# Optimization experiments

Hardware: AMD Instinct MI355X
Metric: run time of the kernel (lower is better)

The kernel has to match this reference:

```python
import jax, jax.numpy as jnp
import numpy as np

E = 4_194_304
N_COMPANY = 100_000
N_CAUSE, N_COURT, N_RES = 200, 50, 10
D_CA, D_COURT, D_CATE = 12, 4, 4
D = D_CA + D_COURT + D_CATE  # 20


def setup_inputs() -> dict:
    key = jax.random.key(0)
    ks = jax.random.split(key, 10)
    cause_idx = jax.random.randint(ks[0], (E,), 0, N_CAUSE, dtype=jnp.int32)
    court_idx = jax.random.randint(ks[1], (E,), 0, N_COURT, dtype=jnp.int32)
    cate_idx = jax.random.randint(ks[2], (E,), 0, N_RES, dtype=jnp.int32)
    seg_ids = jnp.sort(jax.random.randint(ks[3], (E,), 0, N_COMPANY, dtype=jnp.int32))
    time_interval = jax.random.uniform(ks[4], (E,), dtype=jnp.float32) * 365.0
    # learned parameters (nn.Embedding default init ~ N(0,1); Linear ~ U)
    ca_table = jax.random.normal(ks[5], (N_CAUSE, D_CA), dtype=jnp.float32)
    court_table = jax.random.normal(ks[6], (N_COURT, D_COURT), dtype=jnp.float32)
    cate_table = jax.random.normal(ks[7], (N_RES, D_CATE), dtype=jnp.float32)
    lim = 1.0 / np.sqrt(D)
    proj_w = jax.random.uniform(ks[8], (D, D), dtype=jnp.float32, minval=-lim, maxval=lim)
    decay_w = jax.random.uniform(ks[9], (), dtype=jnp.float32, minval=0.5, maxval=1.5)
    return {
        "cause_idx": cause_idx, "court_idx": court_idx, "cate_idx": cate_idx,
        "seg_ids": seg_ids, "time_interval": time_interval,
        "ca_table": ca_table, "court_table": court_table, "cate_table": cate_table,
        "proj_w": proj_w, "decay_w": decay_w,
    }


def reference(cause_idx, court_idx, cate_idx, seg_ids, time_interval,
              ca_table, court_table, cate_table, proj_w, decay_w):
    # per-event categorical embedding gather -> [E, 20]
    risk = jnp.concatenate(
        [ca_table[cause_idx], court_table[court_idx], cate_table[cate_idx]], axis=1)
    # Decayer: learnable scale times inverse-log time decay
    decay = decay_w / jnp.log(jnp.e + time_interval)  # [E]
    # proj(decay * risk): Linear(20, 20, bias=False) -> x @ W^T
    y = jnp.einsum('ed,od->eo', decay[:, None] * risk, proj_w)
    # per-company sum reduction (the original Python loop over companies)
    com_emb = jax.ops.segment_sum(y, seg_ids, num_segments=N_COMPANY,
                                  indices_are_sorted=True)
    return com_emb
```

## Files before the change

kernel.cpp:

```cpp
#include <hip/hip_runtime.h>

#define NCOMP   100000
#define D_CA    12
#define D_COURT 4
#define D_CATE  4
#define D_TOT   20
#define NCAUSE  200
#define NCOURT  50
#define NRES    10
#define LPC     4

__global__ void seg_starts_kernel(const int* __restrict__ seg, int n_events,
                                  int* __restrict__ start) {
    int i = blockIdx.x * blockDim.x + threadIdx.x;
    if (i >= n_events) return;
    const int cur = seg[i];
    const int prev = (i == 0) ? -1 : seg[i - 1];
    for (int c = prev + 1; c <= cur; ++c) start[c] = i;
    if (i == n_events - 1) {
        for (int c = cur + 1; c <= NCOMP; ++c) start[c] = n_events;
    }
}

__global__ __launch_bounds__(256)
void company_emb_kernel(const int* __restrict__ cause_idx,
                        const int* __restrict__ court_idx,
                        const int* __restrict__ cate_idx,
                        const float* __restrict__ time_interval,
                        const float* __restrict__ ca_table,
                        const float* __restrict__ court_table,
                        const float* __restrict__ cate_table,
                        const float* __restrict__ proj_w,
                        const float* __restrict__ decay_w,
                        const int* __restrict__ start,
                        float* __restrict__ out) {
    __shared__ __align__(16) float lds_ca[NCAUSE * D_CA];
    __shared__ __align__(16) float lds_court[NCOURT * D_COURT];
    __shared__ __align__(16) float lds_cate[NRES * D_CATE];
    __shared__ __align__(16) float lds_w[D_TOT * D_TOT];

    for (int i = threadIdx.x; i < NCAUSE * D_CA; i += 256) lds_ca[i] = ca_table[i];
    for (int i = threadIdx.x; i < NCOURT * D_COURT; i += 256) lds_court[i] = court_table[i];
    for (int i = threadIdx.x; i < NRES * D_CATE; i += 256) lds_cate[i] = cate_table[i];
    for (int i = threadIdx.x; i < D_TOT * D_TOT; i += 256) lds_w[i] = proj_w[i];
    __syncthreads();

    const float dw = decay_w[0];
    const int tid = blockIdx.x * 256 + threadIdx.x;
    const int c = tid >> 2;
    const int sub = threadIdx.x & (LPC - 1);
    if (c >= NCOMP) return;

    const int s0 = start[c];
    const int s1 = start[c + 1];

    float acc[D_TOT];
#pragma unroll
    for (int d = 0; d < D_TOT; ++d) acc[d] = 0.0f;

    for (int i = s0 + sub; i < s1; i += LPC) {
        const int ca = cause_idx[i];
        const int co = court_idx[i];
        const int ct = cate_idx[i];
        const float t = time_interval[i];
        const float decay = __fdividef(dw, __logf(2.718281828459045f + t));

        const float4* car = (const float4*)(lds_ca + ca * D_CA);
        const float4 a0 = car[0];
        const float4 a1 = car[1];
        const float4 a2 = car[2];
        const float4 b0 = *(const float4*)(lds_court + co * D_COURT);
        const float4 c0 = *(const float4*)(lds_cate + ct * D_CATE);

        acc[0]  += decay * a0.x;  acc[1]  += decay * a0.y;
        acc[2]  += decay * a0.z;  acc[3]  += decay * a0.w;
        acc[4]  += decay * a1.x;  acc[5]  += decay * a1.y;
        acc[6]  += decay * a1.z;  acc[7]  += decay * a1.w;
        acc[8]  += decay * a2.x;  acc[9]  += decay * a2.y;
        acc[10] += decay * a2.z;  acc[11] += decay * a2.w;
        acc[12] += decay * b0.x;  acc[13] += decay * b0.y;
        acc[14] += decay * b0.z;  acc[15] += decay * b0.w;
        acc[16] += decay * c0.x;  acc[17] += decay * c0.y;
        acc[18] += decay * c0.z;  acc[19] += decay * c0.w;
    }

#pragma unroll
    for (int d = 0; d < D_TOT; ++d) {
        float v = acc[d];
        v += __shfl_xor(v, 1);
        v += __shfl_xor(v, 2);
        acc[d] = v;
    }

#pragma unroll
    for (int k = 0; k < 5; ++k) {
        const int o = sub * 5 + k;
        float s = 0.0f;
#pragma unroll
        for (int d = 0; d < D_TOT; ++d) s += acc[d] * lds_w[o * D_TOT + d];
        out[c * D_TOT + o] = s;
    }
}

extern "C" void kernel_launch(void* const* d_in, const int* in_sizes, int n_in,
                              void* d_out, int out_size, void* d_ws, size_t ws_size,
                              hipStream_t stream) {
    const int* cause_idx = (const int*)d_in[0];
    const int* court_idx = (const int*)d_in[1];
    const int* cate_idx  = (const int*)d_in[2];
    const int* seg_ids   = (const int*)d_in[3];
    const float* time_interval = (const float*)d_in[4];
    const float* ca_table      = (const float*)d_in[5];
    const float* court_table   = (const float*)d_in[6];
    const float* cate_table    = (const float*)d_in[7];
    const float* proj_w        = (const float*)d_in[8];
    const float* decay_w       = (const float*)d_in[9];
    float* out = (float*)d_out;
    const int n_events = in_sizes[0];

    int* start = (int*)d_ws;

    {
        const int blocks = (n_events + 255) / 256;
        seg_starts_kernel<<<blocks, 256, 0, stream>>>(seg_ids, n_events, start);
    }
    {
        const int groups = NCOMP;
        const int blocks = (groups * LPC + 255) / 256;
        company_emb_kernel<<<blocks, 256, 0, stream>>>(
            cause_idx, court_idx, cate_idx, time_interval,
            ca_table, court_table, cate_table, proj_w, decay_w,
            start, out);
    }
}
```

Measured before the change: 156.3 us.

## Fuse segment-start search into main kernel via per-block binary search

Removes the separate segment-start kernel, which read all of seg_ids and wrote a start array. Each block now binary-searches seg_ids for the boundaries of its 32 companies and keeps them in shared memory. Lanes per company go from 4 to 8, and the event loop is unrolled by two to keep more loads in flight. The cost is a serial chain of about 22 dependent global loads per block before any event work begins, plus a shuffle reduction stage widened to eight lanes.

```diff
diff --git a/kernel.cpp b/kernel.cpp
--- a/kernel.cpp
+++ b/kernel.cpp
@@ -8,93 +8,98 @@
 #define NCAUSE  200
 #define NCOURT  50
 #define NRES    10
-#define LPC     4
-
-__global__ void seg_starts_kernel(const int* __restrict__ seg, int n_events,
-                                  int* __restrict__ start) {
-    int i = blockIdx.x * blockDim.x + threadIdx.x;
-    if (i >= n_events) return;
-    const int cur = seg[i];
-    const int prev = (i == 0) ? -1 : seg[i - 1];
-    for (int c = prev + 1; c <= cur; ++c) start[c] = i;
-    if (i == n_events - 1) {
-        for (int c = cur + 1; c <= NCOMP; ++c) start[c] = n_events;
-    }
-}
+#define LPC     8
+#define CPB     32
 
 __global__ __launch_bounds__(256)
-void company_emb_kernel(const int* __restrict__ cause_idx,
-                        const int* __restrict__ court_idx,
-                        const int* __restrict__ cate_idx,
-                        const float* __restrict__ time_interval,
-                        const float* __restrict__ ca_table,
-                        const float* __restrict__ court_table,
-                        const float* __restrict__ cate_table,
-                        const float* __restrict__ proj_w,
-                        const float* __restrict__ decay_w,
-                        const int* __restrict__ start,
-                        float* __restrict__ out) {
+void fused_company_kernel(const int* __restrict__ cause_idx,
+                          const int* __restrict__ court_idx,
+                          const int* __restrict__ cate_idx,
+                          const int* __restrict__ seg_ids,
+                          const float* __restrict__ time_interval,
+                          const float* __restrict__ ca_table,
+                          const float* __restrict__ court_table,
+                          const float* __restrict__ cate_table,
+                          const float* __restrict__ proj_w,
+                          const float* __restrict__ decay_w,
+                          int n_events,
+                          float* __restrict__ out) {
     __shared__ __align__(16) float lds_ca[NCAUSE * D_CA];
     __shared__ __align__(16) float lds_court[NCOURT * D_COURT];
     __shared__ __align__(16) float lds_cate[NRES * D_CATE];
     __shared__ __align__(16) float lds_w[D_TOT * D_TOT];
+    __shared__ int lds_start[CPB + 1];
 
     for (int i = threadIdx.x; i < NCAUSE * D_CA; i += 256) lds_ca[i] = ca_table[i];
     for (int i = threadIdx.x; i < NCOURT * D_COURT; i += 256) lds_court[i] = court_table[i];
     for (int i = threadIdx.x; i < NRES * D_CATE; i += 256) lds_cate[i] = cate_table[i];
     for (int i = threadIdx.x; i < D_TOT * D_TOT; i += 256) lds_w[i] = proj_w[i];
+
+    if (threadIdx.x <= CPB) {
+        const int c = blockIdx.x * CPB + threadIdx.x;
+        int lo = 0, hi = n_events;
+        while (lo < hi) {
+            const int mid = (lo + hi) >> 1;
+            if (seg_ids[mid] < c) lo = mid + 1; else hi = mid;
+        }
+        lds_start[threadIdx.x] = lo;
+    }
     __syncthreads();
 
     const float dw = decay_w[0];
-    const int tid = blockIdx.x * 256 + threadIdx.x;
-    const int c = tid >> 2;
+    const int g   = threadIdx.x >> 3;
     const int sub = threadIdx.x & (LPC - 1);
-    if (c >= NCOMP) return;
-
-    const int s0 = start[c];
-    const int s1 = start[c + 1];
+    const int c   = blockIdx.x * CPB + g;
+    const int s0  = lds_start[g];
+    const int s1  = lds_start[g + 1];
 
     float acc[D_TOT];
 #pragma unroll
     for (int d = 0; d < D_TOT; ++d) acc[d] = 0.0f;
 
-    for (int i = s0 + sub; i < s1; i += LPC) {
-        const int ca = cause_idx[i];
-        const int co = court_idx[i];
-        const int ct = cate_idx[i];
-        const float t = time_interval[i];
-        const float decay = __fdividef(dw, __logf(2.718281828459045f + t));
+#define EV_BODY(I)                                                           \
+    {                                                                        \
+        const int   ca = cause_idx[I];                                       \
+        const int   co = court_idx[I];                                       \
+        const int   ct = cate_idx[I];                                        \
+        const float t  = time_interval[I];                                   \
+        const float dec = __fdividef(dw, __logf(2.718281828459045f + t));    \
+        const float4* car = (const float4*)(lds_ca + ca * D_CA);             \
+        const float4 a0 = car[0];                                            \
+        const float4 a1 = car[1];                                            \
+        const float4 a2 = car[2];                                            \
+        const float4 b0 = *(const float4*)(lds_court + co * D_COURT);        \
+        const float4 c0 = *(const float4*)(lds_cate + ct * D_CATE);          \
+        acc[0]  += dec * a0.x;  acc[1]  += dec * a0.y;                       \
+        acc[2]  += dec * a0.z;  acc[3]  += dec * a0.w;                       \
+        acc[4]  += dec * a1.x;  acc[5]  += dec * a1.y;                       \
+        acc[6]  += dec * a1.z;  acc[7]  += dec * a1.w;                       \
+        acc[8]  += dec * a2.x;  acc[9]  += dec * a2.y;                       \
+        acc[10] += dec * a2.z;  acc[11] += dec * a2.w;                       \
+        acc[12] += dec * b0.x;  acc[13] += dec * b0.y;                       \
+        acc[14] += dec * b0.z;  acc[15] += dec * b0.w;                       \
+        acc[16] += dec * c0.x;  acc[17] += dec * c0.y;                       \
+        acc[18] += dec * c0.z;  acc[19] += dec * c0.w;                       \
+    }
 
-        const float4* car = (const float4*)(lds_ca + ca * D_CA);
-        const float4 a0 = car[0];
-        const float4 a1 = car[1];
-        const float4 a2 = car[2];
-        const float4 b0 = *(const float4*)(lds_court + co * D_COURT);
-        const float4 c0 = *(const float4*)(lds_cate + ct * D_CATE);
-
-        acc[0]  += decay * a0.x;  acc[1]  += decay * a0.y;
-        acc[2]  += decay * a0.z;  acc[3]  += decay * a0.w;
-        acc[4]  += decay * a1.x;  acc[5]  += decay * a1.y;
-        acc[6]  += decay * a1.z;  acc[7]  += decay * a1.w;
-        acc[8]  += decay * a2.x;  acc[9]  += decay * a2.y;
-        acc[10] += decay * a2.z;  acc[11] += decay * a2.w;
-        acc[12] += decay * b0.x;  acc[13] += decay * b0.y;
-        acc[14] += decay * b0.z;  acc[15] += decay * b0.w;
-        acc[16] += decay * c0.x;  acc[17] += decay * c0.y;
-        acc[18] += decay * c0.z;  acc[19] += decay * c0.w;
+    int i = s0 + sub;
+    for (; i + LPC < s1; i += 2 * LPC) {
+        EV_BODY(i);
+        EV_BODY(i + LPC);
     }
+    if (i < s1) EV_BODY(i);
+#undef EV_BODY
 
 #pragma unroll
     for (int d = 0; d < D_TOT; ++d) {
         float v = acc[d];
         v += __shfl_xor(v, 1);
         v += __shfl_xor(v, 2);
+        v += __shfl_xor(v, 4);
         acc[d] = v;
     }
 
-#pragma unroll
-    for (int k = 0; k < 5; ++k) {
-        const int o = sub * 5 + k;
+    for (int o = sub; o < D_TOT; o += LPC) {
         float s = 0.0f;
 #pragma unroll
         for (int d = 0; d < D_TOT; ++d) s += acc[d] * lds_w[o * D_TOT + d];
@@ -118,18 +123,9 @@
     float* out = (float*)d_out;
     const int n_events = in_sizes[0];
 
-    int* start = (int*)d_ws;
-
-    {
-        const int blocks = (n_events + 255) / 256;
-        seg_starts_kernel<<<blocks, 256, 0, stream>>>(seg_ids, n_events, start);
-    }
-    {
-        const int groups = NCOMP;
-        const int blocks = (groups * LPC + 255) / 256;
-        company_emb_kernel<<<blocks, 256, 0, stream>>>(
-            cause_idx, court_idx, cate_idx, time_interval,
-            ca_table, court_table, cate_table, proj_w, decay_w,
-            start, out);
-    }
+    const int blocks = NCOMP / CPB;
+    fused_company_kernel<<<blocks, 256, 0, stream>>>(
+        cause_idx, court_idx, cate_idx, seg_ids, time_interval,
+        ca_table, court_table, cate_table, proj_w, decay_w,
+        n_events, out);
 }
```

After: 148.9 us. 4.7% less time.
